# Kernel tuning notes

Hardware: AMD Instinct MI355X
Metric: run time of the kernel (lower is better)

## Reference

```python
import jax, jax.numpy as jnp
import numpy as np

VOCAB, TYPES, SEQ, EMB, HID, HEADS, HDIM, FFN = 30000, 2, 512, 128, 4096, 64, 64, 16384


def layer_norm(x, g, b, eps=1e-12):
    m = jnp.mean(x, axis=-1, keepdims=True)
    v = jnp.mean(jnp.square(x - m), axis=-1, keepdims=True)
    return (x - m) * jax.lax.rsqrt(v + eps) * g + b


def gelu_tanh(x):
    # 0.5*x*(1+tanh(sqrt(2/pi)*(x+0.044715*x^3))) -- matches the traced graph
    return 0.5 * x * (1.0 + jnp.tanh(0.7978845608028654 * (x + 0.044715 * x * x * x)))


def setup_inputs() -> dict:
    key = jax.random.key(0)
    ks = jax.random.split(key, 16)
    s = 0.02
    inp = {
        'word_emb': jax.random.normal(ks[0], (VOCAB, EMB), jnp.float32) * s,
        'tok_emb': jax.random.normal(ks[1], (TYPES, EMB), jnp.float32) * s,
        'pos_emb': jax.random.normal(ks[2], (SEQ, EMB), jnp.float32) * s,
        'ln0_g': jnp.ones((EMB,), jnp.float32), 'ln0_b': jnp.zeros((EMB,), jnp.float32),
        'W_proj': jax.random.normal(ks[3], (HID, EMB), jnp.float32) * s,
        'b_proj': jnp.zeros((HID,), jnp.float32),
        'Wq': jax.random.normal(ks[4], (HID, HID), jnp.float32) * s,
        'bq': jnp.zeros((HID,), jnp.float32),
        'Wk': jax.random.normal(ks[5], (HID, HID), jnp.float32) * s,
        'bk': jnp.zeros((HID,), jnp.float32),
        'Wv': jax.random.normal(ks[6], (HID, HID), jnp.float32) * s,
        'bv': jnp.zeros((HID,), jnp.float32),
        'Wo': jax.random.normal(ks[7], (HID, HID), jnp.float32) * s,
        'bo': jnp.zeros((HID,), jnp.float32),
        'ln1_g': jnp.ones((HID,), jnp.float32), 'ln1_b': jnp.zeros((HID,), jnp.float32),
        'W_ff1': jax.random.normal(ks[8], (FFN, HID), jnp.float32) * s,
        'b_ff1': jnp.zeros((FFN,), jnp.float32),
        'W_ff2': jax.random.normal(ks[9], (HID, FFN), jnp.float32) * s,
        'b_ff2': jnp.zeros((HID,), jnp.float32),
        'ln2_g': jnp.ones((HID,), jnp.float32), 'ln2_b': jnp.zeros((HID,), jnp.float32),
        'input_ids': jax.random.randint(ks[10], (1, SEQ), 0, VOCAB, jnp.int64 if jax.config.jax_enable_x64 else jnp.int32),
        'token_type_ids': jnp.zeros((SEQ,), jnp.int32),
        'position_ids': jnp.arange(SEQ, dtype=jnp.int32),
    }
    return inp


def reference(word_emb, tok_emb, pos_emb, ln0_g, ln0_b, W_proj, b_proj,
              Wq, bq, Wk, bk, Wv, bv, Wo, bo, ln1_g, ln1_b,
              W_ff1, b_ff1, W_ff2, b_ff2, ln2_g, ln2_b,
              input_ids, token_type_ids, position_ids):
    B, S = input_ids.shape
    # --- embeddings (dim 128) + LayerNorm ---
    e = (word_emb[input_ids]
         + tok_emb[jnp.broadcast_to(token_type_ids[None, :], (B, S))]
         + pos_emb[position_ids][None, :, :])  # [B,S,EMB]
    h_e = layer_norm(e, ln0_g, ln0_b)
    # additive mask from an all-ones attention mask: (1-1)*-10000 == 0
    mask = (1.0 - jnp.ones((B, 1, 1, S), jnp.float32)) * -10000.0
    # --- embedding -> hidden projection ---
    hidden = h_e @ W_proj.T + b_proj  # [B,S,HID]
    # --- self-attention ---
    def split_heads(x):
        return x.reshape(B, S, HEADS, HDIM).transpose(0, 2, 1, 3)  # [B,H,S,D]
    q = split_heads(hidden @ Wq.T + bq)
    k = split_heads(hidden @ Wk.T + bk)
    v = split_heads(hidden @ Wv.T + bv)
    scores = jnp.einsum('bhqd,bhkd->bhqk', q, k) / 8.0 + mask  # [B,H,S,S]
    probs = jax.nn.softmax(scores, axis=-1)
    ctx = jnp.einsum('bhqk,bhkd->bhqd', probs, v)  # [B,H,S,D]
    ctx = ctx.transpose(0, 2, 1, 3).reshape(B, S, HID)
    attn_out = ctx @ Wo.T + bo
    h1 = layer_norm(hidden + attn_out, ln1_g, ln1_b)
    # --- FFN with tanh-GELU ---
    ff = gelu_tanh(h1 @ W_ff1.T + b_ff1) @ W_ff2.T + b_ff2
    h2 = layer_norm(ff + h1, ln2_g, ln2_b)
    return h2
```

## Files before the change

kernel.cpp:

```cpp
#include <hip/hip_runtime.h>
#include <hip/hip_bf16.h>
#include <cmath>

typedef __bf16 bf16_t;
typedef bf16_t bf16x8 __attribute__((ext_vector_type(8)));
typedef float f32x4 __attribute__((ext_vector_type(4)));

__device__ __forceinline__ f32x4 zero4(){ f32x4 z; z[0]=0.f; z[1]=0.f; z[2]=0.f; z[3]=0.f; return z; }

__device__ __forceinline__ bf16x8 cvt8(float4 a, float4 b){
  bf16x8 r;
  r[0]=(bf16_t)a.x; r[1]=(bf16_t)a.y; r[2]=(bf16_t)a.z; r[3]=(bf16_t)a.w;
  r[4]=(bf16_t)b.x; r[5]=(bf16_t)b.y; r[6]=(bf16_t)b.z; r[7]=(bf16_t)b.w;
  return r;
}

__device__ __forceinline__ float gelu_tanh_f(float x){
  float x3 = x*x*x;
  return 0.5f*x*(1.0f + tanhf(0.7978845608028654f*(x + 0.044715f*x3)));
}

__device__ __forceinline__ int swz_col(int row, int col){
  return (col & ~31) | (((((col>>3)&3) ^ ((row>>1)&3)))<<3) | (col&7);
}

#if defined(__has_builtin)
#if __has_builtin(__builtin_amdgcn_global_load_lds)
#define HAS_GLDS 1
#endif
#endif

__device__ __forceinline__ void glds16(const void* g, void* l){
#ifdef HAS_GLDS
  __builtin_amdgcn_global_load_lds(
      (const __attribute__((address_space(1))) unsigned int*)g,
      (__attribute__((address_space(3))) unsigned int*)l, 16, 0, 0);
#else
  *(float4*)((char*)l + (threadIdx.x & 63)*16) = *(const float4*)g;
#endif
}

template<int EPI>
__device__ __forceinline__ void gemm_body(
    const bf16_t* __restrict__ A, const float* __restrict__ Wt,
    const float* __restrict__ biast,
    float* __restrict__ Cf, bf16_t* __restrict__ Cb,
    int Nc, int K, int kt0, int ktn, int brow, int ccol0)
{
  __shared__ __align__(16) bf16_t As[3][256*32];
  __shared__ __align__(16) bf16_t Bs[2][128*40];

  const int tid  = threadIdx.x;
  const int lane = tid & 63;
  const int wave = tid >> 6;
  const int wr = wave >> 1, wc = wave & 1;
  const int ca = ((lane>>4) ^ ((lane>>1)&3))*8;

  const bf16_t* srcA = A + (size_t)(brow + (tid>>2))*K + (tid&3)*8;
  const float*  srcB = Wt + (size_t)(tid>>2)*K + (tid&3)*8;

  auto issueA = [&](int buf, int kt){
    bf16_t* dA = &As[buf][wave*512];
    glds16(srcA + (size_t)kt*32,                  dA);
    glds16(srcA + (size_t)128*K + (size_t)kt*32,  dA + 4096);
  };
  auto loadB = [&](int kt, float4* g){
    const float4* p = (const float4*)(srcB + (size_t)kt*32);
    g[0]=p[0]; g[1]=p[1];
  };
  auto writeB = [&](int buf, const float4* g){
    bf16_t* d = &Bs[buf][(tid>>2)*40 + (tid&3)*8];
    *(bf16x8*)d = cvt8(g[0], g[1]);
  };

  f32x4 acc[4][4];
  #pragma unroll
  for (int m=0;m<4;m++)
    #pragma unroll
    for (int n=0;n<4;n++) acc[m][n] = zero4();

  auto ck = [&](int x){ return kt0 + (x < ktn ? x : ktn-1); };

  float4 sB[2];
  issueA(0, ck(0));
  issueA(1, ck(1));
  {
    float4 g[2];
    loadB(ck(0), g);
    writeB(0, g);
  }
  loadB(ck(1), sB);
  asm volatile("s_waitcnt lgkmcnt(0)" ::: "memory");
  __builtin_amdgcn_s_barrier();

  for (int t=0; t<ktn; ++t){
    const int ra = t % 3, rb = t & 1;
    issueA((t+2)%3, ck(t+2));
    float4 gn[2];
    loadB(ck(t+2), gn);

    bf16x8 af[4], bfr[4];
    #pragma unroll
    for (int m=0;m<4;m++)
      af[m] = *(const bf16x8*)&As[ra][(wr*64 + m*16 + (lane&15))*32 + ca];
    #pragma unroll
    for (int n=0;n<4;n++)
      bfr[n] = *(const bf16x8*)&Bs[rb][(wc*64 + n*16 + (lane&15))*40 + (lane>>4)*8];
    #pragma unroll
    for (int m=0;m<4;m++)
      #pragma unroll
      for (int n=0;n<4;n++)
        acc[m][n] = __builtin_amdgcn_mfma_f32_16x16x32_bf16(af[m], bfr[n], acc[m][n], 0,0,0);

    writeB((t+1)&1, sB);
    sB[0]=gn[0]; sB[1]=gn[1];
    asm volatile("s_waitcnt lgkmcnt(0)" ::: "memory");
    __builtin_amdgcn_s_barrier();
  }

  #pragma unroll
  for (int m=0;m<4;m++){
    #pragma unroll
    for (int n=0;n<4;n++){
      const int col = wc*64 + n*16 + (lane&15);
      const float bv = biast ? biast[col] : 0.f;
      #pragma unroll
      for (int r=0;r<4;r++){
        const int gm = brow + wr*64 + m*16 + (lane>>4)*4 + r;
        float v = acc[m][n][r] + bv;
        if (EPI & 8) v = gelu_tanh_f(v);
        if (EPI & 1) Cf[(size_t)gm*Nc + ccol0 + col] = v;
        if (EPI & 2) Cb[(size_t)gm*Nc + ccol0 + col] = (bf16_t)v;
        if (EPI & 4) Cb[(size_t)gm*Nc + swz_col(gm, ccol0 + col)] = (bf16_t)v;
      }
    }
  }
}

template<int EPI>
__global__ __launch_bounds__(512,4) void gemm_kernel(
    const bf16_t* __restrict__ A, const float* __restrict__ W,
    const float* __restrict__ bias,
    float* __restrict__ Cf, bf16_t* __restrict__ Cb, int N, int K, int nt, int nz)
{
  const int lin = blockIdx.x;
  const int r = lin & 7;
  const int t = lin >> 3;
  const int m = t & 1;
  const int o = r + 8*(t>>1);
  const int n_tile = o % nt;
  const int z = o / nt;
  const int ktn = (K>>5) / nz;
  const float* b = (z==0 && bias) ? bias + n_tile*128 : nullptr;
  gemm_body<EPI>(A, W + (size_t)(n_tile*128)*K, b,
                 (EPI&1) ? Cf + (size_t)z*512*N : nullptr, Cb,
                 N, K, z*ktn, ktn, m*256, n_tile*128);
}

__global__ __launch_bounds__(512,4) void gemm_qkv_kernel(
    const bf16_t* __restrict__ A,
    const float* __restrict__ W0, const float* __restrict__ W1, const float* __restrict__ W2,
    const float* __restrict__ b0, const float* __restrict__ b1, const float* __restrict__ b2,
    float* __restrict__ Cf)
{
  const int lin = blockIdx.x;
  const int r = lin & 7;
  const int t = lin >> 3;
  const int m = t & 1;
  const int o = r + 8*(t>>1);
  const int n_tile = o % 96;
  const int z = o / 96;
  const int which = n_tile >> 5;
  const int lc = (n_tile & 31) * 128;
  const float* W    = (which==0) ? W0 : ((which==1) ? W1 : W2);
  const float* bia  = (which==0) ? b0 : ((which==1) ? b1 : b2);
  const float* b = (z==0) ? bia + lc : nullptr;
  gemm_body<1>(A, W + (size_t)lc*4096, b,
               Cf + (size_t)z*512*12288, nullptr,
               12288, 4096, z*64, 64, m*256, n_tile*128);
}

__global__ __launch_bounds__(256) void reduce_qkv_kernel(
    const float* __restrict__ p, bf16_t* __restrict__ q,
    bf16_t* __restrict__ k, bf16_t* __restrict__ v)
{
  const size_t plane = (size_t)512*12288;
  const int i = (blockIdx.x*256 + threadIdx.x)*8;
  float4 a0 = *(const float4*)(p+i),       a1 = *(const float4*)(p+i+4);
  float4 c0 = *(const float4*)(p+plane+i), c1 = *(const float4*)(p+plane+i+4);
  a0.x+=c0.x; a0.y+=c0.y; a0.z+=c0.z; a0.w+=c0.w;
  a1.x+=c1.x; a1.y+=c1.y; a1.z+=c1.z; a1.w+=c1.w;
  bf16x8 val = cvt8(a0, a1);
  const int row = i / 12288;
  const int col = i - row*12288;
  bf16_t* dst = (col<4096) ? q : ((col<8192) ? k : v);
  *(bf16x8*)(dst + (size_t)row*4096 + (col & 4095)) = val;
}

__global__ __launch_bounds__(256) void reduce_gelu_kernel(
    const float* __restrict__ p, bf16_t* __restrict__ out)
{
  const size_t plane = (size_t)512*16384;
  const int i = (blockIdx.x*256 + threadIdx.x)*8;
  float4 a0 = *(const float4*)(p+i),       a1 = *(const float4*)(p+i+4);
  float4 c0 = *(const float4*)(p+plane+i), c1 = *(const float4*)(p+plane+i+4);
  a0.x=gelu_tanh_f(a0.x+c0.x); a0.y=gelu_tanh_f(a0.y+c0.y);
  a0.z=gelu_tanh_f(a0.z+c0.z); a0.w=gelu_tanh_f(a0.w+c0.w);
  a1.x=gelu_tanh_f(a1.x+c1.x); a1.y=gelu_tanh_f(a1.y+c1.y);
  a1.z=gelu_tanh_f(a1.z+c1.z); a1.w=gelu_tanh_f(a1.w+c1.w);
  const int row = i >> 14;
  const int col = i & 16383;
  *(bf16x8*)(out + (size_t)row*16384 + (size_t)swz_col(row, col)) = cvt8(a0, a1);
}

__global__ void attn_kernel(
    const bf16_t* __restrict__ q, const bf16_t* __restrict__ k,
    const bf16_t* __restrict__ v, bf16_t* __restrict__ ctx)
{
  constexpr int HID = 4096;
  const int qblk = blockIdx.x, head = blockIdx.y;
  const int tid = threadIdx.x, lane = tid & 63, wave = tid >> 6;

  __shared__ __align__(16) bf16_t Ks[128][72];
  __shared__ __align__(16) bf16_t Vt[64][136];
  __shared__ __align__(16) bf16_t Ps[4][16][136];

  bf16x8 qf[2];
  const int qrow0 = qblk*64 + wave*16;
  #pragma unroll
  for (int ks=0;ks<2;ks++)
    qf[ks] = *(const bf16x8*)(q + (size_t)(qrow0 + (lane&15))*HID + head*64 + ks*32 + (lane>>4)*8);

  f32x4 o[4];
  float mrow[4], lrow[4];
  #pragma unroll
  for (int n=0;n<4;n++) o[n] = zero4();
  #pragma unroll
  for (int r=0;r<4;r++){ mrow[r] = -1e30f; lrow[r] = 0.f; }

  for (int t=0; t<4; ++t){
    __syncthreads();
    #pragma unroll
    for (int i=0;i<4;i++){
      int s = tid + i*256; int row = s>>3; int c0 = (s&7)*8;
      *(bf16x8*)&Ks[row][c0] = *(const bf16x8*)(k + (size_t)(t*128+row)*HID + head*64 + c0);
    }
    #pragma unroll
    for (int i=0;i<4;i++){
      int s = tid + i*256; int row = s>>3; int c0 = (s&7)*8;
      bf16x8 vv = *(const bf16x8*)(v + (size_t)(t*128+row)*HID + head*64 + c0);
      #pragma unroll
      for (int e=0;e<8;e++) Vt[c0+e][row] = vv[e];
    }
    __syncthreads();

    f32x4 sa[8];
    #pragma unroll
    for (int n=0;n<8;n++) sa[n] = zero4();
    #pragma unroll
    for (int ks=0;ks<2;ks++)
      #pragma unroll
      for (int n=0;n<8;n++){
        bf16x8 kf = *(const bf16x8*)&Ks[n*16 + (lane&15)][ks*32 + (lane>>4)*8];
        sa[n] = __builtin_amdgcn_mfma_f32_16x16x32_bf16(qf[ks], kf, sa[n], 0,0,0);
      }

    float pm[4], rs[4];
    #pragma unroll
    for (int r=0;r<4;r++){
      float mx = sa[0][r];
      #pragma unroll
      for (int n=1;n<8;n++) mx = fmaxf(mx, sa[n][r]);
      pm[r] = mx * 0.125f;
      #pragma unroll
      for (int off=1; off<16; off<<=1) pm[r] = fmaxf(pm[r], __shfl_xor(pm[r], off));
      float mnew  = fmaxf(mrow[r], pm[r]);
      float alpha = __expf(mrow[r] - mnew);
      mrow[r] = mnew; lrow[r] *= alpha;
      #pragma unroll
      for (int n=0;n<4;n++) o[n][r] *= alpha;
      rs[r] = 0.f;
    }
    #pragma unroll
    for (int n=0;n<8;n++)
      #pragma unroll
      for (int r=0;r<4;r++){
        float p = __expf(sa[n][r]*0.125f - mrow[r]);
        rs[r] += p;
        Ps[wave][(lane>>4)*4 + r][n*16 + (lane&15)] = (bf16_t)p;
      }
    #pragma unroll
    for (int r=0;r<4;r++){
      #pragma unroll
      for (int off=1; off<16; off<<=1) rs[r] += __shfl_xor(rs[r], off);
      lrow[r] += rs[r];
    }

    #pragma unroll
    for (int ksv=0;ksv<4;ksv++){
      bf16x8 pf = *(const bf16x8*)&Ps[wave][lane&15][ksv*32 + (lane>>4)*8];
      #pragma unroll
      for (int n=0;n<4;n++){
        bf16x8 vf = *(const bf16x8*)&Vt[n*16 + (lane&15)][ksv*32 + (lane>>4)*8];
        o[n] = __builtin_amdgcn_mfma_f32_16x16x32_bf16(pf, vf, o[n], 0,0,0);
      }
    }
  }

  #pragma unroll
  for (int n=0;n<4;n++)
    #pragma unroll
    for (int r=0;r<4;r++){
      const int gm = qrow0 + (lane>>4)*4 + r;
      const int gd = head*64 + n*16 + (lane&15);
      ctx[(size_t)gm*HID + swz_col(gm, gd)] = (bf16_t)(o[n][r] / lrow[r]);
    }
}

template<int NP>
__global__ __launch_bounds__(256) void ln_final_kernel(
    const float* __restrict__ p, const float* __restrict__ resid,
    const float* __restrict__ bias,
    const float* __restrict__ g, const float* __restrict__ b,
    float* __restrict__ yf, bf16_t* __restrict__ yb)
{
  __shared__ float red[4];
  const int row = blockIdx.x, tid = threadIdx.x;
  const size_t base = (size_t)row * 4096;
  const size_t ps = (size_t)512*4096;
  float vals[16];
  float s = 0.f;
  #pragma unroll
  for (int i=0;i<16;i++){
    int c = i*256 + tid;
    float t = bias[c] + resid[base+c];
    #pragma unroll
    for (int z=0;z<NP;z++) t += p[(size_t)z*ps + base + c];
    vals[i] = t; s += t;
  }
  #pragma unroll
  for (int off=1; off<64; off<<=1) s += __shfl_xor(s, off);
  if (!(tid&63)) red[tid>>6] = s;
  __syncthreads();
  const float mean = (red[0]+red[1]+red[2]+red[3]) * (1.0f/4096.0f);
  __syncthreads();
  float s2 = 0.f;
  #pragma unroll
  for (int i=0;i<16;i++){ float d = vals[i]-mean; s2 += d*d; }
  #pragma unroll
  for (int off=1; off<64; off<<=1) s2 += __shfl_xor(s2, off);
  if (!(tid&63)) red[tid>>6] = s2;
  __syncthreads();
  const float rstd = rsqrtf((red[0]+red[1]+red[2]+red[3])*(1.0f/4096.0f) + 1e-12f);
  #pragma unroll
  for (int i=0;i<16;i++){
    int c = i*256 + tid;
    float y = (vals[i]-mean)*rstd*g[c] + b[c];
    yf[base+c] = y;
    if (yb) yb[base + swz_col(row, c)] = (bf16_t)y;
  }
}

__global__ __launch_bounds__(128) void embed_ln_kernel(
    const float* __restrict__ we, const float* __restrict__ te, const float* __restrict__ pe,
    const float* __restrict__ g, const float* __restrict__ bb,
    const int* __restrict__ ids, const int* __restrict__ tt, const int* __restrict__ pos,
    bf16_t* __restrict__ out)
{
  __shared__ float red[2];
  const int row = blockIdx.x, tid = threadIdx.x;
  float e = we[(size_t)ids[row]*128 + tid] + te[(size_t)tt[row]*128 + tid] + pe[(size_t)pos[row]*128 + tid];
  float s = e;
  #pragma unroll
  for (int off=1; off<64; off<<=1) s += __shfl_xor(s, off);
  if (!(tid&63)) red[tid>>6] = s;
  __syncthreads();
  const float mean = (red[0]+red[1]) * (1.0f/128.0f);
  __syncthreads();
  float d = e - mean;
  float s2 = d*d;
  #pragma unroll
  for (int off=1; off<64; off<<=1) s2 += __shfl_xor(s2, off);
  if (!(tid&63)) red[tid>>6] = s2;
  __syncthreads();
  const float var = (red[0]+red[1]) * (1.0f/128.0f);
  float y = d * rsqrtf(var + 1e-12f) * g[tid] + bb[tid];
  out[(size_t)row*128 + swz_col(row, tid)] = (bf16_t)y;
}

extern "C" void kernel_launch(void* const* d_in, const int* in_sizes, int n_in,
                              void* d_out, int out_size, void* d_ws, size_t ws_size,
                              hipStream_t stream) {
  const float* we   = (const float*)d_in[0];
  const float* te   = (const float*)d_in[1];
  const float* pe   = (const float*)d_in[2];
  const float* ln0g = (const float*)d_in[3];
  const float* ln0b = (const float*)d_in[4];
  const float* Wp   = (const float*)d_in[5];
  const float* bp   = (const float*)d_in[6];
  const float* Wq   = (const float*)d_in[7];
  const float* bq   = (const float*)d_in[8];
  const float* Wk   = (const float*)d_in[9];
  const float* bk   = (const float*)d_in[10];
  const float* Wv   = (const float*)d_in[11];
  const float* bv   = (const float*)d_in[12];
  const float* Wo   = (const float*)d_in[13];
  const float* bo   = (const float*)d_in[14];
  const float* ln1g = (const float*)d_in[15];
  const float* ln1b = (const float*)d_in[16];
  const float* Wf1  = (const float*)d_in[17];
  const float* bf1  = (const float*)d_in[18];
  const float* Wf2  = (const float*)d_in[19];
  const float* bf2  = (const float*)d_in[20];
  const float* ln2g = (const float*)d_in[21];
  const float* ln2b = (const float*)d_in[22];
  const int* ids = (const int*)d_in[23];
  const int* tt  = (const int*)d_in[24];
  const int* pos = (const int*)d_in[25];
  float* out = (float*)d_out;

  float* ws = (float*)d_ws;
  const size_t M1 = (size_t)1024*1024;
  float* hidden_f32 = ws;
  float* h1_f32     = ws + 2*M1;
  float* part       = ws + 4*M1;
  bf16_t* b16 = (bf16_t*)(ws + 20*M1);
  bf16_t* hid_b  = b16;
  bf16_t* h1_b   = b16 + 2*M1;
  bf16_t* ctxb   = b16 + 4*M1;
  bf16_t* qb     = b16 + 6*M1;
  bf16_t* kb     = b16 + 8*M1;
  bf16_t* vb     = b16 + 10*M1;
  bf16_t* he_b   = b16 + 12*M1;
  bf16_t* gelu_b = b16 + 4*M1;

  embed_ln_kernel<<<dim3(512),dim3(128),0,stream>>>(we,te,pe,ln0g,ln0b,ids,tt,pos,he_b);
  gemm_kernel<5><<<dim3(64),dim3(512),0,stream>>>(he_b, Wp, bp, hidden_f32, hid_b, 4096, 128, 32, 1);
  gemm_qkv_kernel<<<dim3(384),dim3(512),0,stream>>>(hid_b, Wq,Wk,Wv, bq,bk,bv, part);
  reduce_qkv_kernel<<<dim3(3072),dim3(256),0,stream>>>(part, qb, kb, vb);
  attn_kernel<<<dim3(8,64),dim3(256),0,stream>>>(qb, kb, vb, ctxb);
  gemm_kernel<1><<<dim3(512),dim3(512),0,stream>>>(ctxb, Wo, nullptr, part, nullptr, 4096, 4096, 32, 8);
  ln_final_kernel<8><<<dim3(512),dim3(256),0,stream>>>(part, hidden_f32, bo, ln1g, ln1b, h1_f32, h1_b);
  gemm_kernel<1><<<dim3(512),dim3(512),0,stream>>>(h1_b, Wf1, bf1, part, nullptr, 16384, 4096, 128, 2);
  reduce_gelu_kernel<<<dim3(4096),dim3(256),0,stream>>>(part, gelu_b);
  gemm_kernel<1><<<dim3(512),dim3(512),0,stream>>>(gelu_b, Wf2, nullptr, part, nullptr, 4096, 16384, 32, 8);
  ln_final_kernel<8><<<dim3(512),dim3(256),0,stream>>>(part, h1_f32, bf2, ln2g, ln2b, out, nullptr);
}
```

Before: 496.4 us.

## Store split-K GEMM partials in bf16 and deepen QKV split-K to four

Split-K partial sums from all GEMMs are now written as bf16 instead of fp32, and the reduce/LayerNorm kernels read bf16 partials and accumulate in fp32. The QKV GEMM goes from two to four K splits (768 blocks) for more parallelism. This halves the partial-buffer write and read traffic. The cost is lost precision in the partial sums, which may affect accuracy against the reference.

```diff
diff --git a/kernel.cpp b/kernel.cpp
--- a/kernel.cpp
+++ b/kernel.cpp
@@ -153,7 +153,8 @@
   const int ktn = (K>>5) / nz;
   const float* b = (z==0 && bias) ? bias + n_tile*128 : nullptr;
   gemm_body<EPI>(A, W + (size_t)(n_tile*128)*K, b,
-                 (EPI&1) ? Cf + (size_t)z*512*N : nullptr, Cb,
+                 (EPI&1) ? Cf + (size_t)z*512*N : nullptr,
+                 (EPI&6) ? Cb + (size_t)z*512*N : nullptr,
                  N, K, z*ktn, ktn, m*256, n_tile*128);
 }
 
@@ -161,7 +162,7 @@
     const bf16_t* __restrict__ A,
     const float* __restrict__ W0, const float* __restrict__ W1, const float* __restrict__ W2,
     const float* __restrict__ b0, const float* __restrict__ b1, const float* __restrict__ b2,
-    float* __restrict__ Cf)
+    bf16_t* __restrict__ Cb)
 {
   const int lin = blockIdx.x;
   const int r = lin & 7;
@@ -175,22 +176,29 @@
   const float* W    = (which==0) ? W0 : ((which==1) ? W1 : W2);
   const float* bia  = (which==0) ? b0 : ((which==1) ? b1 : b2);
   const float* b = (z==0) ? bia + lc : nullptr;
-  gemm_body<1>(A, W + (size_t)lc*4096, b,
-               Cf + (size_t)z*512*12288, nullptr,
-               12288, 4096, z*64, 64, m*256, n_tile*128);
+  gemm_body<2>(A, W + (size_t)lc*4096, b, nullptr,
+               Cb + (size_t)z*512*12288,
+               12288, 4096, z*32, 32, m*256, n_tile*128);
 }
 
 __global__ __launch_bounds__(256) void reduce_qkv_kernel(
-    const float* __restrict__ p, bf16_t* __restrict__ q,
+    const bf16_t* __restrict__ p, bf16_t* __restrict__ q,
     bf16_t* __restrict__ k, bf16_t* __restrict__ v)
 {
   const size_t plane = (size_t)512*12288;
   const int i = (blockIdx.x*256 + threadIdx.x)*8;
-  float4 a0 = *(const float4*)(p+i),       a1 = *(const float4*)(p+i+4);
-  float4 c0 = *(const float4*)(p+plane+i), c1 = *(const float4*)(p+plane+i+4);
-  a0.x+=c0.x; a0.y+=c0.y; a0.z+=c0.z; a0.w+=c0.w;
-  a1.x+=c1.x; a1.y+=c1.y; a1.z+=c1.z; a1.w+=c1.w;
-  bf16x8 val = cvt8(a0, a1);
+  float s[8];
+  #pragma unroll
+  for (int e=0;e<8;e++) s[e] = 0.f;
+  #pragma unroll
+  for (int z=0;z<4;z++){
+    bf16x8 w = *(const bf16x8*)(p + (size_t)z*plane + i);
+    #pragma unroll
+    for (int e=0;e<8;e++) s[e] += (float)w[e];
+  }
+  bf16x8 val;
+  #pragma unroll
+  for (int e=0;e<8;e++) val[e] = (bf16_t)s[e];
   const int row = i / 12288;
   const int col = i - row*12288;
   bf16_t* dst = (col<4096) ? q : ((col<8192) ? k : v);
@@ -198,19 +206,18 @@
 }
 
 __global__ __launch_bounds__(256) void reduce_gelu_kernel(
-    const float* __restrict__ p, bf16_t* __restrict__ out)
+    const bf16_t* __restrict__ p, bf16_t* __restrict__ out)
 {
   const size_t plane = (size_t)512*16384;
   const int i = (blockIdx.x*256 + threadIdx.x)*8;
-  float4 a0 = *(const float4*)(p+i),       a1 = *(const float4*)(p+i+4);
-  float4 c0 = *(const float4*)(p+plane+i), c1 = *(const float4*)(p+plane+i+4);
-  a0.x=gelu_tanh_f(a0.x+c0.x); a0.y=gelu_tanh_f(a0.y+c0.y);
-  a0.z=gelu_tanh_f(a0.z+c0.z); a0.w=gelu_tanh_f(a0.w+c0.w);
-  a1.x=gelu_tanh_f(a1.x+c1.x); a1.y=gelu_tanh_f(a1.y+c1.y);
-  a1.z=gelu_tanh_f(a1.z+c1.z); a1.w=gelu_tanh_f(a1.w+c1.w);
+  bf16x8 w0 = *(const bf16x8*)(p + i);
+  bf16x8 w1 = *(const bf16x8*)(p + plane + i);
+  bf16x8 val;
+  #pragma unroll
+  for (int e=0;e<8;e++) val[e] = (bf16_t)gelu_tanh_f((float)w0[e] + (float)w1[e]);
   const int row = i >> 14;
   const int col = i & 16383;
-  *(bf16x8*)(out + (size_t)row*16384 + (size_t)swz_col(row, col)) = cvt8(a0, a1);
+  *(bf16x8*)(out + (size_t)row*16384 + (size_t)swz_col(row, col)) = val;
 }
 
 __global__ void attn_kernel(
@@ -319,7 +326,7 @@
 
 template<int NP>
 __global__ __launch_bounds__(256) void ln_final_kernel(
-    const float* __restrict__ p, const float* __restrict__ resid,
+    const bf16_t* __restrict__ p, const float* __restrict__ resid,
     const float* __restrict__ bias,
     const float* __restrict__ g, const float* __restrict__ b,
     float* __restrict__ yf, bf16_t* __restrict__ yb)
@@ -335,7 +342,7 @@
     int c = i*256 + tid;
     float t = bias[c] + resid[base+c];
     #pragma unroll
-    for (int z=0;z<NP;z++) t += p[(size_t)z*ps + base + c];
+    for (int z=0;z<NP;z++) t += (float)p[(size_t)z*ps + base + c];
     vals[i] = t; s += t;
   }
   #pragma unroll
@@ -423,26 +430,26 @@
   const size_t M1 = (size_t)1024*1024;
   float* hidden_f32 = ws;
   float* h1_f32     = ws + 2*M1;
-  float* part       = ws + 4*M1;
-  bf16_t* b16 = (bf16_t*)(ws + 20*M1);
-  bf16_t* hid_b  = b16;
-  bf16_t* h1_b   = b16 + 2*M1;
-  bf16_t* ctxb   = b16 + 4*M1;
-  bf16_t* qb     = b16 + 6*M1;
-  bf16_t* kb     = b16 + 8*M1;
-  bf16_t* vb     = b16 + 10*M1;
-  bf16_t* he_b   = b16 + 12*M1;
-  bf16_t* gelu_b = b16 + 4*M1;
+  bf16_t* b16 = (bf16_t*)(ws + 4*M1);
+  bf16_t* part_b = b16;
+  bf16_t* hid_b  = b16 + 26*M1;
+  bf16_t* h1_b   = b16 + 28*M1;
+  bf16_t* ctxb   = b16 + 30*M1;
+  bf16_t* qb     = b16 + 32*M1;
+  bf16_t* kb     = b16 + 34*M1;
+  bf16_t* vb     = b16 + 36*M1;
+  bf16_t* he_b   = b16 + 38*M1;
+  bf16_t* gelu_b = b16 + 30*M1;
 
   embed_ln_kernel<<<dim3(512),dim3(128),0,stream>>>(we,te,pe,ln0g,ln0b,ids,tt,pos,he_b);
   gemm_kernel<5><<<dim3(64),dim3(512),0,stream>>>(he_b, Wp, bp, hidden_f32, hid_b, 4096, 128, 32, 1);
-  gemm_qkv_kernel<<<dim3(384),dim3(512),0,stream>>>(hid_b, Wq,Wk,Wv, bq,bk,bv, part);
-  reduce_qkv_kernel<<<dim3(3072),dim3(256),0,stream>>>(part, qb, kb, vb);
+  gemm_qkv_kernel<<<dim3(768),dim3(512),0,stream>>>(hid_b, Wq,Wk,Wv, bq,bk,bv, part_b);
+  reduce_qkv_kernel<<<dim3(3072),dim3(256),0,stream>>>(part_b, qb, kb, vb);
   attn_kernel<<<dim3(8,64),dim3(256),0,stream>>>(qb, kb, vb, ctxb);
-  gemm_kernel<1><<<dim3(512),dim3(512),0,stream>>>(ctxb, Wo, nullptr, part, nullptr, 4096, 4096, 32, 8);
-  ln_final_kernel<8><<<dim3(512),dim3(256),0,stream>>>(part, hidden_f32, bo, ln1g, ln1b, h1_f32, h1_b);
-  gemm_kernel<1><<<dim3(512),dim3(512),0,stream>>>(h1_b, Wf1, bf1, part, nullptr, 16384, 4096, 128, 2);
-  reduce_gelu_kernel<<<dim3(4096),dim3(256),0,stream>>>(part, gelu_b);
-  gemm_kernel<1><<<dim3(512),dim3(512),0,stream>>>(gelu_b, Wf2, nullptr, part, nullptr, 4096, 16384, 32, 8);
-  ln_final_kernel<8><<<dim3(512),dim3(256),0,stream>>>(part, h1_f32, bf2, ln2g, ln2b, out, nullptr);
-}
+  gemm_kernel<2><<<dim3(512),dim3(512),0,stream>>>(ctxb, Wo, nullptr, nullptr, part_b, 4096, 4096, 32, 8);
+  ln_final_kernel<8><<<dim3(512),dim3(256),0,stream>>>(part_b, hidden_f32, bo, ln1g, ln1b, h1_f32, h1_b);
+  gemm_kernel<2><<<dim3(512),dim3(512),0,stream>>>(h1_b, Wf1, bf1, nullptr, part_b, 16384, 4096, 128, 2);
+  reduce_gelu_kernel<<<dim3(4096),dim3(256),0,stream>>>(part_b, gelu_b);
+  gemm_kernel<2><<<dim3(512),dim3(512),0,stream>>>(gelu_b, Wf2, nullptr, nullptr, part_b, 4096, 16384, 32, 8);
+  ln_final_kernel<8><<<dim3(512),dim3(256),0,stream>>>(part_b, h1_f32, bf2, ln2g, ln2b, out, nullptr);
+}
```

New measurement: 465.8 us. 6.2% less time.
